# Kernel tuning notes

Hardware: AMD Instinct MI355X
Metric: run time of the kernel (lower is better)

## Reference

```python
import jax, jax.numpy as jnp
import numpy as np

N_NODES = 100000
N_EDGES = 1600000
D_IN = 64
D_H = 64


def setup_inputs() -> dict:
    key = jax.random.key(0)
    ks = jax.random.split(key, 8)
    inp = {
        "in_feat": jax.random.normal(ks[0], (N_NODES, D_IN), dtype=jnp.float32),
        "src": jax.random.randint(ks[1], (N_EDGES,), 0, N_NODES, dtype=jnp.int64)
        if jax.config.jax_enable_x64
        else jax.random.randint(ks[1], (N_EDGES,), 0, N_NODES).astype(jnp.int32),
        "dst": jax.random.randint(ks[2], (N_EDGES,), 0, N_NODES).astype(jnp.int32),
        "W_self1": jax.random.normal(ks[3], (D_H, D_IN), dtype=jnp.float32) * 0.1,
        "W_neigh1": jax.random.normal(ks[4], (D_H, D_IN), dtype=jnp.float32) * 0.1,
        "b1": jnp.zeros((D_H,), dtype=jnp.float32),
        "W_self2": jax.random.normal(ks[5], (D_H, D_H), dtype=jnp.float32) * 0.1,
        "W_neigh2": jax.random.normal(ks[6], (D_H, D_H), dtype=jnp.float32) * 0.1,
        "b2": jnp.zeros((D_H,), dtype=jnp.float32),
    }
    inp["src"] = inp["src"].astype(jnp.int32)
    return inp


def _sage_mean(x, src, dst, W_self, W_neigh, b, n_nodes):
    # mean aggregation over incoming edges: gather src feats, segment-sum at dst
    msg_sum = jax.ops.segment_sum(x[src], dst, num_segments=n_nodes)  # [N, D]
    deg = jax.ops.segment_sum(jnp.ones_like(dst, dtype=x.dtype), dst, num_segments=n_nodes)
    h_neigh = msg_sum / jnp.maximum(deg, 1.0)[:, None]
    # DGL SAGEConv: fc_self(h) + fc_neigh(h_neigh) + bias
    return x @ W_self.T + h_neigh @ W_neigh.T + b


def reference(in_feat, src, dst, W_self1, W_neigh1, b1, W_self2, W_neigh2, b2):
    n = in_feat.shape[0]
    h = _sage_mean(in_feat, src, dst, W_self1, W_neigh1, b1, n)
    # dropout in eval mode is identity; then relu
    h = jax.nn.relu(h)
    h = _sage_mean(h, src, dst, W_self2, W_neigh2, b2, n)
    return h
```

## Files before the change

### kernel.cpp

```cpp
#include <hip/hip_runtime.h>

#define NN 100000
#define NE 1600000
#define NROWS 100032
#define CAP 48
#define ZOFF (NN * 64)
#define NRANGES 128
#define NRANGE2 782
#define BINCAP2 120
#define SCAT_EPB 8192
#define NCHUNK 196
#define CAST_BLKS 6250
#define WCAT_BLKS 64
#define AGG_BLKS 1563

typedef __attribute__((ext_vector_type(8))) short short8;
typedef __attribute__((ext_vector_type(4))) float float4v;
typedef __attribute__((ext_vector_type(4))) int int4v;

__device__ inline unsigned short f2bf(float f)
{
    union { float f; unsigned u; } v; v.f = f;
    unsigned r = v.u + 0x7FFF + ((v.u >> 16) & 1);
    return (unsigned short)(r >> 16);
}
__device__ inline float bf2f(unsigned short h)
{
    union { unsigned u; float f; } v; v.u = ((unsigned)h) << 16; return v.f;
}

__global__ __launch_bounds__(256) void zbin_kernel(
    const int* __restrict__ src, const int* __restrict__ dst,
    const float* __restrict__ Ws1, const float* __restrict__ Wn1,
    const float* __restrict__ Ws2, const float* __restrict__ Wn2,
    unsigned short* __restrict__ XF,
    unsigned short* __restrict__ W1, unsigned short* __restrict__ W2,
    int* __restrict__ bins, int* __restrict__ bcnt)
{
    const int b = blockIdx.x;
    const int tid = threadIdx.x;
    if (b < NCHUNK) {
        __shared__ int lcnt[NRANGES];
        for (int i = tid; i < NRANGES; i += 256) lcnt[i] = 0;
        __syncthreads();
        const int base = b * SCAT_EPB;
        #pragma unroll
        for (int k = 0; k < 8; ++k) {
            int e = base + (k * 256 + tid) * 4;
            if (e < NE) {
                int4v s4 = __builtin_nontemporal_load((const int4v*)(src + e));
                int4v d4 = __builtin_nontemporal_load((const int4v*)(dst + e));
                #pragma unroll
                for (int r = 0; r < 4; ++r) {
                    int d = d4[r];
                    int g = (unsigned)d / NRANGE2;
                    int lpos = atomicAdd(&lcnt[g], 1);
                    if (lpos < BINCAP2)
                        __builtin_nontemporal_store(
                            ((d - g * NRANGE2) << 17) | s4[r],
                            bins + (size_t)(b * NRANGES + g) * BINCAP2 + lpos);
                }
            }
        }
        __syncthreads();
        for (int i = tid; i < NRANGES; i += 256)
            bcnt[b * NRANGES + i] = min(lcnt[i], BINCAP2);
    } else if (b < NCHUNK + WCAT_BLKS) {
        int id = (b - NCHUNK) * 256 + tid;
        int l = id >> 13;
        int r = id & 8191;
        int o = r >> 7, k = r & 127;
        const float* Ws = l ? Ws2 : Ws1;
        const float* Wn = l ? Wn2 : Wn1;
        float v = (k < 64) ? Ws[o * 64 + k] : Wn[o * 64 + (k - 64)];
        (l ? W2 : W1)[r] = f2bf(v);
    } else {
        ushort4 z; z.x = 0; z.y = 0; z.z = 0; z.w = 0;
        for (int i = tid; i < 512; i += 256)
            *(ushort4*)(XF + (size_t)NN * 64 + i * 4) = z;
    }
}

__global__ __launch_bounds__(256) void prep_kernel(
    const float* __restrict__ x,
    const int* __restrict__ bins, const int* __restrict__ bcnt,
    unsigned short* __restrict__ XF,
    int* __restrict__ cur, int* __restrict__ colb)
{
    const int b = blockIdx.x;
    const int tid = threadIdx.x;
    if (b < NRANGES) {
        __shared__ int cnt[NRANGE2];
        const int lo = b * NRANGE2;
        for (int i = tid; i < NRANGE2; i += 256) cnt[i] = 0;
        __syncthreads();

        const int grp = tid >> 6;
        const int i = tid & 63;

        int c = grp;
        int m = bcnt[c * NRANGES + b];
        const int* seg = bins + (size_t)(c * NRANGES + b) * BINCAP2;
        int va = (i < m) ? __builtin_nontemporal_load(seg + i) : -1;
        int vb = (i + 64 < m) ? __builtin_nontemporal_load(seg + i + 64) : -1;

        for (int cn = grp + 4; cn < NCHUNK; cn += 4) {
            int m2 = bcnt[cn * NRANGES + b];
            const int* seg2 = bins + (size_t)(cn * NRANGES + b) * BINCAP2;
            int wa = (i < m2) ? __builtin_nontemporal_load(seg2 + i) : -1;
            int wb = (i + 64 < m2) ? __builtin_nontemporal_load(seg2 + i + 64) : -1;
            if (va >= 0) {
                int dr = va >> 17;
                int p = atomicAdd(&cnt[dr], 1);
                if (p < CAP) colb[(size_t)(lo + dr) * CAP + p] = (va & 0x1FFFF) << 6;
            }
            if (vb >= 0) {
                int dr = vb >> 17;
                int p = atomicAdd(&cnt[dr], 1);
                if (p < CAP) colb[(size_t)(lo + dr) * CAP + p] = (vb & 0x1FFFF) << 6;
            }
            va = wa; vb = wb;
        }
        if (va >= 0) {
            int dr = va >> 17;
            int p = atomicAdd(&cnt[dr], 1);
            if (p < CAP) colb[(size_t)(lo + dr) * CAP + p] = (va & 0x1FFFF) << 6;
        }
        if (vb >= 0) {
            int dr = vb >> 17;
            int p = atomicAdd(&cnt[dr], 1);
            if (p < CAP) colb[(size_t)(lo + dr) * CAP + p] = (vb & 0x1FFFF) << 6;
        }
        __syncthreads();
        const int nd = min(NRANGE2, NN - lo);
        for (int i2 = tid; i2 < nd; i2 += 256) cur[lo + i2] = cnt[i2];
    } else {
        int t = (b - NRANGES) * 256 + tid;
        int n = t >> 4;
        int k4 = (t & 15) * 4;
        float4v v = __builtin_nontemporal_load(
            (const float4v*)(x + (size_t)n * 64 + k4));
        ushort4 o;
        o.x = f2bf(v[0]); o.y = f2bf(v[1]); o.z = f2bf(v[2]); o.w = f2bf(v[3]);
        *(ushort4*)(XF + (size_t)n * 64 + k4) = o;
    }
}

template <int LAYER1>
__global__ __launch_bounds__(256) void aggdense_kernel(
    const unsigned short* __restrict__ XIN,
    const int* __restrict__ cur,
    const int* __restrict__ colb,
    const unsigned short* __restrict__ Wcat,
    const float* __restrict__ bias,
    unsigned short* __restrict__ xout,
    float* __restrict__ fout)
{
    __shared__ __align__(16) unsigned short HN[64 * 72];
    const int tid = threadIdx.x;
    const int wave = tid >> 6;
    const int lane = tid & 63;
    const int g = lane >> 4;
    const int q = lane & 15;
    const int nbase = blockIdx.x * 64 + wave * 16;

    int cntv = (lane < 16 && nbase + lane < NN) ? cur[nbase + lane] : 0;

    int cnt_nx = __shfl(cntv, 0, 64);
    int cc_nx = min(cnt_nx, CAP);
    int ci_nx = (nbase < NN && lane < cc_nx) ? colb[(size_t)nbase * CAP + lane] : ZOFF;

    for (int i = 0; i < 16; ++i) {
        int n = nbase + i;
        int cnt = cnt_nx, cc = cc_nx, ci = ci_nx;
        if (i < 15) {
            cnt_nx = __shfl(cntv, i + 1, 64);
            cc_nx = min(cnt_nx, CAP);
            ci_nx = ((n + 1) < NN && lane < cc_nx)
                      ? colb[(size_t)(n + 1) * CAP + lane] : ZOFF;
        }
        if (n < NN) {
            float a0 = 0.f, a1 = 0.f, a2 = 0.f, a3 = 0.f;
            for (int t = 0; t < cc; t += 16) {
                int i0 = __shfl(ci, t + g, 64);
                int i1 = __shfl(ci, t + 4 + g, 64);
                int i2 = __shfl(ci, t + 8 + g, 64);
                int i3 = __shfl(ci, t + 12 + g, 64);
                ushort4 v0 = *(const ushort4*)(XIN + i0 + q * 4);
                ushort4 v1 = *(const ushort4*)(XIN + i1 + q * 4);
                ushort4 v2 = *(const ushort4*)(XIN + i2 + q * 4);
                ushort4 v3 = *(const ushort4*)(XIN + i3 + q * 4);
                a0 += bf2f(v0.x) + bf2f(v1.x) + bf2f(v2.x) + bf2f(v3.x);
                a1 += bf2f(v0.y) + bf2f(v1.y) + bf2f(v2.y) + bf2f(v3.y);
                a2 += bf2f(v0.z) + bf2f(v1.z) + bf2f(v2.z) + bf2f(v3.z);
                a3 += bf2f(v0.w) + bf2f(v1.w) + bf2f(v2.w) + bf2f(v3.w);
            }
            a0 += __shfl_xor(a0, 16, 64); a0 += __shfl_xor(a0, 32, 64);
            a1 += __shfl_xor(a1, 16, 64); a1 += __shfl_xor(a1, 32, 64);
            a2 += __shfl_xor(a2, 16, 64); a2 += __shfl_xor(a2, 32, 64);
            a3 += __shfl_xor(a3, 16, 64); a3 += __shfl_xor(a3, 32, 64);
            float rdeg = 1.0f / fmaxf((float)cnt, 1.0f);
            if (g == 0) {
                ushort4 o;
                o.x = f2bf(a0 * rdeg); o.y = f2bf(a1 * rdeg);
                o.z = f2bf(a2 * rdeg); o.w = f2bf(a3 * rdeg);
                *(ushort4*)(&HN[(wave * 16 + i) * 72 + q * 4]) = o;
            }
        }
    }
    __syncthreads();

    const int mrow = lane & 15;
    const int kb = lane >> 4;
    const int row0 = nbase;

    short8 a[4];
    {
        const short* ax = (const short*)XIN + (size_t)(row0 + mrow) * 64 + kb * 8;
        const short* ah = (const short*)HN + (wave * 16 + mrow) * 72 + kb * 8;
        a[0] = *(const short8*)(ax);
        a[1] = *(const short8*)(ax + 32);
        a[2] = *(const short8*)(ah);
        a[3] = *(const short8*)(ah + 32);
    }

    float4v acc[4];
    #pragma unroll
    for (int c = 0; c < 4; ++c) acc[c] = (float4v){0.f, 0.f, 0.f, 0.f};

    #pragma unroll
    for (int c = 0; c < 4; ++c) {
        const short* brow = (const short*)Wcat + (c * 16 + mrow) * 128 + kb * 8;
        #pragma unroll
        for (int i = 0; i < 4; ++i) {
            short8 bfr = *(const short8*)(brow + i * 32);
            acc[c] = __builtin_amdgcn_mfma_f32_16x16x32_bf16(a[i], bfr, acc[c], 0, 0, 0);
        }
    }

    const int rbase = row0 + (lane >> 4) * 4;
    #pragma unroll
    for (int c = 0; c < 4; ++c) {
        int o = c * 16 + mrow;
        float bv = bias[o];
        #pragma unroll
        for (int r = 0; r < 4; ++r) {
            int node = rbase + r;
            float val = acc[c][r] + bv;
            if (LAYER1) {
                float h = (node < NN) ? fmaxf(val, 0.f) : 0.f;
                xout[(size_t)node * 64 + o] = f2bf(h);
            } else {
                if (node < NN) fout[(size_t)node * 64 + o] = val;
            }
        }
    }
}

extern "C" void kernel_launch(void* const* d_in, const int* in_sizes, int n_in,
                              void* d_out, int out_size, void* d_ws, size_t ws_size,
                              hipStream_t stream)
{
    const float* in_feat = (const float*)d_in[0];
    const int*   src     = (const int*)d_in[1];
    const int*   dst     = (const int*)d_in[2];
    const float* Ws1     = (const float*)d_in[3];
    const float* Wn1     = (const float*)d_in[4];
    const float* b1      = (const float*)d_in[5];
    const float* Ws2     = (const float*)d_in[6];
    const float* Wn2     = (const float*)d_in[7];
    const float* b2      = (const float*)d_in[8];
    float* out = (float*)d_out;

    int* cur  = (int*)d_ws;
    int* colb = cur + NN;
    unsigned short* XF = (unsigned short*)(colb + (size_t)NN * CAP);
    unsigned short* H1 = XF + (size_t)NROWS * 64;
    unsigned short* W1 = H1 + (size_t)NROWS * 64;
    unsigned short* W2 = W1 + 8192;
    int* bins = (int*)H1;
    int* bcnt = bins + (size_t)NCHUNK * NRANGES * BINCAP2;

    zbin_kernel<<<NCHUNK + WCAT_BLKS + 1, 256, 0, stream>>>(
        src, dst, Ws1, Wn1, Ws2, Wn2, XF, W1, W2, bins, bcnt);

    prep_kernel<<<NRANGES + CAST_BLKS, 256, 0, stream>>>(
        in_feat, bins, bcnt, XF, cur, colb);

    aggdense_kernel<1><<<AGG_BLKS, 256, 0, stream>>>(
        XF, cur, colb, W1, b1, H1, nullptr);

    aggdense_kernel<0><<<AGG_BLKS, 256, 0, stream>>>(
        H1, cur, colb, W2, b2, nullptr, out);
}
```

Before: 244.2 us.

## Fuse all phases into one cooperative persistent kernel with grid syncs

Merges the binning, CSR build, and both aggregation layers into a single cooperative kernel of 1024 blocks separated by grid.sync, with non-cooperative kernels kept as a fallback. It also changes the binning geometry to 256 ranges, 98 chunks of 16K edges and a bin capacity of 112, and folds the feature cast into the binning phase as a grid-stride loop. The phase-1 merge now uses one bin entry per thread across all chunks rather than four wave groups. The aim is to remove inter-kernel launch gaps. In exchange, grid-wide barriers and a capped persistent grid may lower occupancy and parallelism in the aggregation phases.

```diff
diff --git a/kernel.cpp b/kernel.cpp
--- a/kernel.cpp
+++ b/kernel.cpp
@@ -1,18 +1,21 @@
 #include <hip/hip_runtime.h>
+#include <hip/hip_cooperative_groups.h>
+
+namespace cg = cooperative_groups;
 
 #define NN 100000
 #define NE 1600000
 #define NROWS 100032
 #define CAP 48
 #define ZOFF (NN * 64)
-#define NRANGES 128
-#define NRANGE2 782
-#define BINCAP2 120
-#define SCAT_EPB 8192
-#define NCHUNK 196
-#define CAST_BLKS 6250
-#define WCAT_BLKS 64
-#define AGG_BLKS 1563
+#define NRANGES 256
+#define RNG 391
+#define NCHUNK 98
+#define CHUNK 16384
+#define BINCAP 112
+#define GRID_C 1024
+#define AGG_UNITS 1563
+#define FLATN (NN * 16 + 16384 + 512)
 
 typedef __attribute__((ext_vector_type(8))) short short8;
 typedef __attribute__((ext_vector_type(4))) float float4v;
@@ -29,23 +32,23 @@
     union { unsigned u; float f; } v; v.u = ((unsigned)h) << 16; return v.f;
 }
 
-__global__ __launch_bounds__(256) void zbin_kernel(
+__device__ __forceinline__ void phase0_dev(
+    int b, int tid, int nflat,
+    const float* __restrict__ x,
     const int* __restrict__ src, const int* __restrict__ dst,
     const float* __restrict__ Ws1, const float* __restrict__ Wn1,
     const float* __restrict__ Ws2, const float* __restrict__ Wn2,
     unsigned short* __restrict__ XF,
     unsigned short* __restrict__ W1, unsigned short* __restrict__ W2,
-    int* __restrict__ bins, int* __restrict__ bcnt)
-{
-    const int b = blockIdx.x;
-    const int tid = threadIdx.x;
+    int* __restrict__ bins, int* __restrict__ bcnt,
+    int* lcnt)
+{
     if (b < NCHUNK) {
-        __shared__ int lcnt[NRANGES];
         for (int i = tid; i < NRANGES; i += 256) lcnt[i] = 0;
         __syncthreads();
-        const int base = b * SCAT_EPB;
+        const int base = b * CHUNK;
         #pragma unroll
-        for (int k = 0; k < 8; ++k) {
+        for (int k = 0; k < 16; ++k) {
             int e = base + (k * 256 + tid) * 4;
             if (e < NE) {
                 int4v s4 = __builtin_nontemporal_load((const int4v*)(src + e));
@@ -53,116 +56,92 @@
                 #pragma unroll
                 for (int r = 0; r < 4; ++r) {
                     int d = d4[r];
-                    int g = (unsigned)d / NRANGE2;
+                    int g = (unsigned)d / RNG;
                     int lpos = atomicAdd(&lcnt[g], 1);
-                    if (lpos < BINCAP2)
-                        __builtin_nontemporal_store(
-                            ((d - g * NRANGE2) << 17) | s4[r],
-                            bins + (size_t)(b * NRANGES + g) * BINCAP2 + lpos);
+                    if (lpos < BINCAP)
+                        bins[(size_t)(b * NRANGES + g) * BINCAP + lpos] =
+                            ((d - g * RNG) << 17) | s4[r];
                 }
             }
         }
         __syncthreads();
         for (int i = tid; i < NRANGES; i += 256)
-            bcnt[b * NRANGES + i] = min(lcnt[i], BINCAP2);
-    } else if (b < NCHUNK + WCAT_BLKS) {
-        int id = (b - NCHUNK) * 256 + tid;
-        int l = id >> 13;
-        int r = id & 8191;
-        int o = r >> 7, k = r & 127;
-        const float* Ws = l ? Ws2 : Ws1;
-        const float* Wn = l ? Wn2 : Wn1;
-        float v = (k < 64) ? Ws[o * 64 + k] : Wn[o * 64 + (k - 64)];
-        (l ? W2 : W1)[r] = f2bf(v);
+            bcnt[b * NRANGES + i] = min(lcnt[i], BINCAP);
     } else {
-        ushort4 z; z.x = 0; z.y = 0; z.z = 0; z.w = 0;
-        for (int i = tid; i < 512; i += 256)
-            *(ushort4*)(XF + (size_t)NN * 64 + i * 4) = z;
-    }
-}
-
-__global__ __launch_bounds__(256) void prep_kernel(
-    const float* __restrict__ x,
+        for (int u = (b - NCHUNK) * 256 + tid; u < FLATN; u += nflat * 256) {
+            if (u < NN * 16) {
+                int n = u >> 4;
+                int k4 = (u & 15) * 4;
+                float4v v = __builtin_nontemporal_load(
+                    (const float4v*)(x + (size_t)n * 64 + k4));
+                ushort4 o;
+                o.x = f2bf(v[0]); o.y = f2bf(v[1]);
+                o.z = f2bf(v[2]); o.w = f2bf(v[3]);
+                *(ushort4*)(XF + (size_t)n * 64 + k4) = o;
+            } else if (u < NN * 16 + 16384) {
+                int id = u - NN * 16;
+                int l = id >> 13;
+                int r = id & 8191;
+                int o = r >> 7, k = r & 127;
+                const float* Ws = l ? Ws2 : Ws1;
+                const float* Wn = l ? Wn2 : Wn1;
+                float v = (k < 64) ? Ws[o * 64 + k] : Wn[o * 64 + (k - 64)];
+                (l ? W2 : W1)[r] = f2bf(v);
+            } else {
+                int i = u - NN * 16 - 16384;
+                ushort4 z; z.x = 0; z.y = 0; z.z = 0; z.w = 0;
+                *(ushort4*)(XF + (size_t)NN * 64 + i * 4) = z;
+            }
+        }
+    }
+}
+
+__device__ __forceinline__ void phase1_dev(
+    int b, int tid,
     const int* __restrict__ bins, const int* __restrict__ bcnt,
-    unsigned short* __restrict__ XF,
-    int* __restrict__ cur, int* __restrict__ colb)
-{
-    const int b = blockIdx.x;
-    const int tid = threadIdx.x;
-    if (b < NRANGES) {
-        __shared__ int cnt[NRANGE2];
-        const int lo = b * NRANGE2;
-        for (int i = tid; i < NRANGE2; i += 256) cnt[i] = 0;
-        __syncthreads();
-
-        const int grp = tid >> 6;
-        const int i = tid & 63;
-
-        int c = grp;
-        int m = bcnt[c * NRANGES + b];
-        const int* seg = bins + (size_t)(c * NRANGES + b) * BINCAP2;
-        int va = (i < m) ? __builtin_nontemporal_load(seg + i) : -1;
-        int vb = (i + 64 < m) ? __builtin_nontemporal_load(seg + i + 64) : -1;
-
-        for (int cn = grp + 4; cn < NCHUNK; cn += 4) {
-            int m2 = bcnt[cn * NRANGES + b];
-            const int* seg2 = bins + (size_t)(cn * NRANGES + b) * BINCAP2;
-            int wa = (i < m2) ? __builtin_nontemporal_load(seg2 + i) : -1;
-            int wb = (i + 64 < m2) ? __builtin_nontemporal_load(seg2 + i + 64) : -1;
-            if (va >= 0) {
-                int dr = va >> 17;
-                int p = atomicAdd(&cnt[dr], 1);
-                if (p < CAP) colb[(size_t)(lo + dr) * CAP + p] = (va & 0x1FFFF) << 6;
-            }
-            if (vb >= 0) {
-                int dr = vb >> 17;
-                int p = atomicAdd(&cnt[dr], 1);
-                if (p < CAP) colb[(size_t)(lo + dr) * CAP + p] = (vb & 0x1FFFF) << 6;
-            }
-            va = wa; vb = wb;
+    int* __restrict__ cur, int* __restrict__ colb,
+    int* cnt)
+{
+    if (b >= NRANGES) return;
+    const int lo = b * RNG;
+    for (int i = tid; i < RNG; i += 256) cnt[i] = 0;
+    __syncthreads();
+
+    int m0 = bcnt[b];
+    int va = (tid < m0) ? bins[(size_t)b * BINCAP + tid] : -1;
+    for (int c = 1; c <= NCHUNK; ++c) {
+        int vb = -1;
+        if (c < NCHUNK) {
+            int m = bcnt[c * NRANGES + b];
+            vb = (tid < m) ? bins[(size_t)(c * NRANGES + b) * BINCAP + tid] : -1;
         }
         if (va >= 0) {
             int dr = va >> 17;
             int p = atomicAdd(&cnt[dr], 1);
-            if (p < CAP) colb[(size_t)(lo + dr) * CAP + p] = (va & 0x1FFFF) << 6;
-        }
-        if (vb >= 0) {
-            int dr = vb >> 17;
-            int p = atomicAdd(&cnt[dr], 1);
-            if (p < CAP) colb[(size_t)(lo + dr) * CAP + p] = (vb & 0x1FFFF) << 6;
-        }
-        __syncthreads();
-        const int nd = min(NRANGE2, NN - lo);
-        for (int i2 = tid; i2 < nd; i2 += 256) cur[lo + i2] = cnt[i2];
-    } else {
-        int t = (b - NRANGES) * 256 + tid;
-        int n = t >> 4;
-        int k4 = (t & 15) * 4;
-        float4v v = __builtin_nontemporal_load(
-            (const float4v*)(x + (size_t)n * 64 + k4));
-        ushort4 o;
-        o.x = f2bf(v[0]); o.y = f2bf(v[1]); o.z = f2bf(v[2]); o.w = f2bf(v[3]);
-        *(ushort4*)(XF + (size_t)n * 64 + k4) = o;
-    }
+            if (p < CAP)
+                colb[(size_t)(lo + dr) * CAP + p] = (va & 0x1FFFF) << 6;
+        }
+        va = vb;
+    }
+    __syncthreads();
+    const int nd = min(RNG, NN - lo);
+    for (int i = tid; i < nd; i += 256) cur[lo + i] = cnt[i];
 }
 
 template <int LAYER1>
-__global__ __launch_bounds__(256) void aggdense_kernel(
+__device__ __forceinline__ void aggdense_unit(
+    int u, int tid,
     const unsigned short* __restrict__ XIN,
-    const int* __restrict__ cur,
-    const int* __restrict__ colb,
-    const unsigned short* __restrict__ Wcat,
-    const float* __restrict__ bias,
-    unsigned short* __restrict__ xout,
-    float* __restrict__ fout)
-{
-    __shared__ __align__(16) unsigned short HN[64 * 72];
-    const int tid = threadIdx.x;
+    const int* __restrict__ cur, const int* __restrict__ colb,
+    const unsigned short* __restrict__ Wcat, const float* __restrict__ bias,
+    unsigned short* __restrict__ xout, float* __restrict__ fout,
+    unsigned short* HN)
+{
     const int wave = tid >> 6;
     const int lane = tid & 63;
     const int g = lane >> 4;
     const int q = lane & 15;
-    const int nbase = blockIdx.x * 64 + wave * 16;
+    const int nbase = u * 64 + wave * 16;
 
     int cntv = (lane < 16 && nbase + lane < NN) ? cur[nbase + lane] : 0;
 
@@ -238,7 +217,7 @@
         }
     }
 
-    const int rbase = row0 + (lane >> 4) * 4;
+    const int rbase = row0 + kb * 4;
     #pragma unroll
     for (int c = 0; c < 4; ++c) {
         int o = c * 16 + mrow;
@@ -257,6 +236,76 @@
     }
 }
 
+__global__ __launch_bounds__(256, 4) void mega_kernel(
+    const float* __restrict__ x,
+    const int* __restrict__ src, const int* __restrict__ dst,
+    const float* __restrict__ Ws1, const float* __restrict__ Wn1,
+    const float* __restrict__ b1,
+    const float* __restrict__ Ws2, const float* __restrict__ Wn2,
+    const float* __restrict__ b2,
+    float* __restrict__ out,
+    int* __restrict__ cur, int* __restrict__ colb,
+    unsigned short* __restrict__ XF, unsigned short* __restrict__ H1,
+    unsigned short* __restrict__ W1, unsigned short* __restrict__ W2,
+    int* __restrict__ bins, int* __restrict__ bcnt)
+{
+    cg::grid_group grid = cg::this_grid();
+    __shared__ __align__(16) unsigned char smem[64 * 72 * 2];
+    const int b = blockIdx.x;
+    const int tid = threadIdx.x;
+
+    phase0_dev(b, tid, GRID_C - NCHUNK, x, src, dst, Ws1, Wn1, Ws2, Wn2,
+               XF, W1, W2, bins, bcnt, (int*)smem);
+    grid.sync();
+    phase1_dev(b, tid, bins, bcnt, cur, colb, (int*)smem);
+    grid.sync();
+    for (int u = b; u < AGG_UNITS; u += GRID_C) {
+        aggdense_unit<1>(u, tid, XF, cur, colb, W1, b1, H1, nullptr,
+                         (unsigned short*)smem);
+        __syncthreads();
+    }
+    grid.sync();
+    for (int u = b; u < AGG_UNITS; u += GRID_C) {
+        aggdense_unit<0>(u, tid, H1, cur, colb, W2, b2, nullptr, out,
+                         (unsigned short*)smem);
+        __syncthreads();
+    }
+}
+
+__global__ __launch_bounds__(256) void p0_kernel(
+    const float* __restrict__ x,
+    const int* __restrict__ src, const int* __restrict__ dst,
+    const float* __restrict__ Ws1, const float* __restrict__ Wn1,
+    const float* __restrict__ Ws2, const float* __restrict__ Wn2,
+    unsigned short* __restrict__ XF,
+    unsigned short* __restrict__ W1, unsigned short* __restrict__ W2,
+    int* __restrict__ bins, int* __restrict__ bcnt)
+{
+    __shared__ int lcnt[NRANGES];
+    phase0_dev(blockIdx.x, threadIdx.x, GRID_C - NCHUNK, x, src, dst,
+               Ws1, Wn1, Ws2, Wn2, XF, W1, W2, bins, bcnt, lcnt);
+}
+
+__global__ __launch_bounds__(256) void p1_kernel(
+    const int* __restrict__ bins, const int* __restrict__ bcnt,
+    int* __restrict__ cur, int* __restrict__ colb)
+{
+    __shared__ int cnt[RNG];
+    phase1_dev(blockIdx.x, threadIdx.x, bins, bcnt, cur, colb, cnt);
+}
+
+template <int LAYER1>
+__global__ __launch_bounds__(256) void agg_kernel(
+    const unsigned short* __restrict__ XIN,
+    const int* __restrict__ cur, const int* __restrict__ colb,
+    const unsigned short* __restrict__ Wcat, const float* __restrict__ bias,
+    unsigned short* __restrict__ xout, float* __restrict__ fout)
+{
+    __shared__ __align__(16) unsigned short HN[64 * 72];
+    aggdense_unit<LAYER1>(blockIdx.x, threadIdx.x, XIN, cur, colb,
+                          Wcat, bias, xout, fout, HN);
+}
+
 extern "C" void kernel_launch(void* const* d_in, const int* in_sizes, int n_in,
                               void* d_out, int out_size, void* d_ws, size_t ws_size,
                               hipStream_t stream)
@@ -279,17 +328,25 @@
     unsigned short* W1 = H1 + (size_t)NROWS * 64;
     unsigned short* W2 = W1 + 8192;
     int* bins = (int*)H1;
-    int* bcnt = bins + (size_t)NCHUNK * NRANGES * BINCAP2;
-
-    zbin_kernel<<<NCHUNK + WCAT_BLKS + 1, 256, 0, stream>>>(
-        src, dst, Ws1, Wn1, Ws2, Wn2, XF, W1, W2, bins, bcnt);
-
-    prep_kernel<<<NRANGES + CAST_BLKS, 256, 0, stream>>>(
-        in_feat, bins, bcnt, XF, cur, colb);
-
-    aggdense_kernel<1><<<AGG_BLKS, 256, 0, stream>>>(
-        XF, cur, colb, W1, b1, H1, nullptr);
-
-    aggdense_kernel<0><<<AGG_BLKS, 256, 0, stream>>>(
-        H1, cur, colb, W2, b2, nullptr, out);
-}
+    int* bcnt = bins + (size_t)NCHUNK * NRANGES * BINCAP;
+
+    void* args[] = {
+        (void*)&in_feat, (void*)&src, (void*)&dst,
+        (void*)&Ws1, (void*)&Wn1, (void*)&b1,
+        (void*)&Ws2, (void*)&Wn2, (void*)&b2,
+        (void*)&out,
+        (void*)&cur, (void*)&colb, (void*)&XF, (void*)&H1,
+        (void*)&W1, (void*)&W2, (void*)&bins, (void*)&bcnt
+    };
+    hipError_t err = hipLaunchCooperativeKernel(
+        (void*)mega_kernel, dim3(GRID_C), dim3(256), args, 0, stream);
+    if (err != hipSuccess) {
+        p0_kernel<<<GRID_C, 256, 0, stream>>>(
+            in_feat, src, dst, Ws1, Wn1, Ws2, Wn2, XF, W1, W2, bins, bcnt);
+        p1_kernel<<<NRANGES, 256, 0, stream>>>(bins, bcnt, cur, colb);
+        agg_kernel<1><<<AGG_UNITS, 256, 0, stream>>>(
+            XF, cur, colb, W1, b1, H1, nullptr);
+        agg_kernel<0><<<AGG_UNITS, 256, 0, stream>>>(
+            H1, cur, colb, W2, b2, nullptr, out);
+    }
+}
```

After: 644.0 us. 2.64x slower.
